# Performance work log

Hardware: AMD Instinct MI355X
Metric: run time of the kernel (lower is better)

## Reference

```python
import jax, jax.numpy as jnp
import numpy as np
from jax import lax

SEQ_LEN = 15
LATENT = 16
HIDDEN = 64
OUT = 1
BATCH = 65536


def setup_inputs() -> dict:
    key = jax.random.key(0)
    ks = jax.random.split(key, 11)
    s = lambda *shape: 1.0 / np.sqrt(HIDDEN)
    def u(k, shape):
        return jax.random.uniform(k, shape, jnp.float32, -1.0 / np.sqrt(HIDDEN), 1.0 / np.sqrt(HIDDEN))
    return {
        "z": jax.random.normal(ks[0], (BATCH, LATENT), jnp.float32),
        "Wih0": u(ks[1], (4 * HIDDEN, LATENT)),
        "Whh0": u(ks[2], (4 * HIDDEN, HIDDEN)),
        "bih0": u(ks[3], (4 * HIDDEN,)),
        "bhh0": u(ks[4], (4 * HIDDEN,)),
        "Wih1": u(ks[5], (4 * HIDDEN, HIDDEN)),
        "Whh1": u(ks[6], (4 * HIDDEN, HIDDEN)),
        "bih1": u(ks[7], (4 * HIDDEN,)),
        "bhh1": u(ks[8], (4 * HIDDEN,)),
        "Wfc": u(ks[9], (OUT, HIDDEN)),
        "bfc": u(ks[10], (OUT,)),
    }


def lstm_layer(x, Wih, Whh, bih, bhh):
    # x: [B, T, D]. PyTorch gate order: i, f, g, o.
    B, T, _ = x.shape
    H = Whh.shape[1]
    # precompute input projections for all timesteps: [T, B, 4H]
    x_proj = jnp.einsum('btd,gd->tbg', x, Wih) + (bih + bhh)

    def step(carry, xp):
        h, c = carry
        gates = xp + h @ Whh.T
        i, f, g, o = jnp.split(gates, 4, axis=-1)
        i = jax.nn.sigmoid(i)
        f = jax.nn.sigmoid(f)
        g = jnp.tanh(g)
        o = jax.nn.sigmoid(o)
        c = f * c + i * g
        h = o * jnp.tanh(c)
        return (h, c), h

    h0 = jnp.zeros((B, H), x.dtype)
    _, ys = lax.scan(step, (h0, h0), x_proj)  # ys: [T, B, H]
    return jnp.swapaxes(ys, 0, 1)  # [B, T, H]


def reference(z, Wih0, Whh0, bih0, bhh0, Wih1, Whh1, bih1, bhh1, Wfc, bfc):
    # z: [B, latent] -> repeat along time: [B, T, latent]
    x = jnp.broadcast_to(z[:, None, :], (z.shape[0], SEQ_LEN, z.shape[1]))
    h1 = lstm_layer(x, Wih0, Whh0, bih0, bhh0)
    # (inter-layer dropout is inactive in eval mode)
    h2 = lstm_layer(h1, Wih1, Whh1, bih1, bhh1)
    return h2 @ Wfc.T + bfc  # [B, T, OUT]
```

## Files before the change

kernel.cpp:

```cpp
#include <hip/hip_runtime.h>

#define TSTEPS 15
#define HID    64
#define LAT    16
#define NBATCH 65536

typedef _Float16 v8h __attribute__((ext_vector_type(8)));
typedef _Float16 v4h __attribute__((ext_vector_type(4)));
typedef float    v4f __attribute__((ext_vector_type(4)));

__device__ __forceinline__ float fast_sig(float x) {
    return __builtin_amdgcn_rcpf(1.0f + __expf(-x));
}
__device__ __forceinline__ float fast_tanh(float x) {
    return 2.0f * __builtin_amdgcn_rcpf(1.0f + __expf(-2.0f * x)) - 1.0f;
}

__device__ __forceinline__ v8h vzero8() {
    v8h v;
#pragma unroll
    for (int i = 0; i < 8; ++i) v[i] = (_Float16)0.0f;
    return v;
}

__global__ __launch_bounds__(512, 2) void lstm2_fused2(
        const float* __restrict__ z,
        const float* __restrict__ Wih0, const float* __restrict__ Whh0,
        const float* __restrict__ bih0, const float* __restrict__ bhh0,
        const float* __restrict__ Wih1, const float* __restrict__ Whh1,
        const float* __restrict__ bih1, const float* __restrict__ bhh1,
        const float* __restrict__ Wfc,  const float* __restrict__ bfc,
        float* __restrict__ out)
{
    __shared__ __align__(16) _Float16 wf[7 * 16 * 64 * 8];
    __shared__ __align__(16) float    bsum[512];
    __shared__ __align__(16) float    wfcs[64];
    __shared__ __align__(16) _Float16 state[8][32 * 72];

    const int tid  = threadIdx.x;
    const int wave = tid >> 6;
    const int lane = tid & 63;
    const int q    = lane >> 4;
    const int c    = lane & 15;
    const int row0 = blockIdx.x * 256 + wave * 32;

#pragma unroll 4
    for (int e = tid; e < 7 * 16 * 64 * 8; e += 512) {
        const int j  = e & 7;
        const int lm = (e >> 3) & 63;
        const int mt = (e >> 9) & 15;
        const int p  = e >> 13;
        const int g  = mt * 16 + (lm & 15);
        const int kk = (lm >> 4) * 8 + j;
        float v;
        if (p == 0)      v = (kk < LAT) ? Wih0[g * LAT + kk] : 0.0f;
        else if (p == 1) v = Whh0[g * HID + kk];
        else if (p == 2) v = Whh0[g * HID + 32 + kk];
        else if (p == 3) v = Wih1[g * HID + kk];
        else if (p == 4) v = Wih1[g * HID + 32 + kk];
        else if (p == 5) v = Whh1[g * HID + kk];
        else             v = Whh1[g * HID + 32 + kk];
        wf[e] = (_Float16)v;
    }
    bsum[tid] = (tid < 256) ? bih0[tid] + bhh0[tid]
                            : bih1[tid - 256] + bhh1[tid - 256];
    if (tid < 64) wfcs[tid] = Wfc[tid];
    __syncthreads();

    _Float16* stW = &state[wave][0];
    const float bfcv = bfc[0];

    v8h zfrag[2];
#pragma unroll
    for (int n = 0; n < 2; ++n) {
        zfrag[n] = vzero8();
        if (q < 2) {
            const float* zp = z + (size_t)(row0 + 16 * n + c) * LAT + q * 8;
            const float4 za = *(const float4*)(zp);
            const float4 zb = *(const float4*)(zp + 4);
            zfrag[n][0] = (_Float16)za.x; zfrag[n][1] = (_Float16)za.y;
            zfrag[n][2] = (_Float16)za.z; zfrag[n][3] = (_Float16)za.w;
            zfrag[n][4] = (_Float16)zb.x; zfrag[n][5] = (_Float16)zb.y;
            zfrag[n][6] = (_Float16)zb.z; zfrag[n][7] = (_Float16)zb.w;
        }
    }

    v8h hf[2][2], gf[2][2];
    float c0s[2][16], c1s[2][16];
#pragma unroll
    for (int n = 0; n < 2; ++n) {
        hf[n][0] = vzero8(); hf[n][1] = vzero8();
        gf[n][0] = vzero8(); gf[n][1] = vzero8();
#pragma unroll
        for (int i = 0; i < 16; ++i) { c0s[n][i] = 0.0f; c1s[n][i] = 0.0f; }
    }

#define AFRAG(pl, mt) (*(const v8h*)&wf[(((pl) * 16 + (mt)) * 64 + lane) * 8])

#pragma unroll 1
    for (int t = 0; t < TSTEPS; ++t) {
        __asm__ __volatile__("" ::: "memory");

#pragma unroll
        for (int a = 0; a < 4; ++a) {
            v4f acc[2][4];
#pragma unroll
            for (int ty = 0; ty < 4; ++ty) {
                const int mt = 4 * ty + a;
                const v4f b  = *(const v4f*)&bsum[64 * ty + 16 * a + 4 * q];
                const v8h a0 = AFRAG(0, mt);
                const v8h a1 = AFRAG(1, mt);
                const v8h a2 = AFRAG(2, mt);
                v4f t0 = __builtin_amdgcn_mfma_f32_16x16x32_f16(a0, zfrag[0], b, 0, 0, 0);
                v4f t1 = __builtin_amdgcn_mfma_f32_16x16x32_f16(a0, zfrag[1], b, 0, 0, 0);
                t0 = __builtin_amdgcn_mfma_f32_16x16x32_f16(a1, hf[0][0], t0, 0, 0, 0);
                t1 = __builtin_amdgcn_mfma_f32_16x16x32_f16(a1, hf[1][0], t1, 0, 0, 0);
                t0 = __builtin_amdgcn_mfma_f32_16x16x32_f16(a2, hf[0][1], t0, 0, 0, 0);
                t1 = __builtin_amdgcn_mfma_f32_16x16x32_f16(a2, hf[1][1], t1, 0, 0, 0);
                acc[0][ty] = t0;
                acc[1][ty] = t1;
            }
#pragma unroll
            for (int n = 0; n < 2; ++n) {
                v4h pk;
#pragma unroll
                for (int r = 0; r < 4; ++r) {
                    const float ig = fast_sig(acc[0][0][r] * 0.0f + ((const v4f*)acc[n])[0][r]);
                    (void)ig;
                }
#pragma unroll
                for (int r = 0; r < 4; ++r) {
                    const float ig = fast_sig(((v4f*)acc[n])[0][r]);
                    const float fg = fast_sig(((v4f*)acc[n])[1][r]);
                    const float gg = fast_tanh(((v4f*)acc[n])[2][r]);
                    const float og = fast_sig(((v4f*)acc[n])[3][r]);
                    const float cc = fg * c0s[n][a * 4 + r] + ig * gg;
                    c0s[n][a * 4 + r] = cc;
                    pk[r] = (_Float16)(og * fast_tanh(cc));
                }
                *(v4h*)&stW[(c + 16 * n) * 72 + 16 * a + 4 * q] = pk;
            }
        }
#pragma unroll
        for (int n = 0; n < 2; ++n) {
            hf[n][0] = *(const v8h*)&stW[(c + 16 * n) * 72 + 8 * q];
            hf[n][1] = *(const v8h*)&stW[(c + 16 * n) * 72 + 32 + 8 * q];
        }

        float p0 = 0.0f, p1 = 0.0f;
#pragma unroll
        for (int a = 0; a < 4; ++a) {
            v4f acc[2][4];
#pragma unroll
            for (int ty = 0; ty < 4; ++ty) {
                const int mt = 4 * ty + a;
                const v4f b  = *(const v4f*)&bsum[256 + 64 * ty + 16 * a + 4 * q];
                const v8h a3 = AFRAG(3, mt);
                const v8h a4 = AFRAG(4, mt);
                const v8h a5 = AFRAG(5, mt);
                const v8h a6 = AFRAG(6, mt);
                v4f t0 = __builtin_amdgcn_mfma_f32_16x16x32_f16(a3, hf[0][0], b, 0, 0, 0);
                v4f t1 = __builtin_amdgcn_mfma_f32_16x16x32_f16(a3, hf[1][0], b, 0, 0, 0);
                t0 = __builtin_amdgcn_mfma_f32_16x16x32_f16(a4, hf[0][1], t0, 0, 0, 0);
                t1 = __builtin_amdgcn_mfma_f32_16x16x32_f16(a4, hf[1][1], t1, 0, 0, 0);
                t0 = __builtin_amdgcn_mfma_f32_16x16x32_f16(a5, gf[0][0], t0, 0, 0, 0);
                t1 = __builtin_amdgcn_mfma_f32_16x16x32_f16(a5, gf[1][0], t1, 0, 0, 0);
                t0 = __builtin_amdgcn_mfma_f32_16x16x32_f16(a6, gf[0][1], t0, 0, 0, 0);
                t1 = __builtin_amdgcn_mfma_f32_16x16x32_f16(a6, gf[1][1], t1, 0, 0, 0);
                acc[0][ty] = t0;
                acc[1][ty] = t1;
            }
            const v4f wv = *(const v4f*)&wfcs[16 * a + 4 * q];
#pragma unroll
            for (int n = 0; n < 2; ++n) {
                v4h pk;
#pragma unroll
                for (int r = 0; r < 4; ++r) {
                    const float ig = fast_sig(((v4f*)acc[n])[0][r]);
                    const float fg = fast_sig(((v4f*)acc[n])[1][r]);
                    const float gg = fast_tanh(((v4f*)acc[n])[2][r]);
                    const float og = fast_sig(((v4f*)acc[n])[3][r]);
                    const float cc = fg * c1s[n][a * 4 + r] + ig * gg;
                    c1s[n][a * 4 + r] = cc;
                    const float hh = og * fast_tanh(cc);
                    pk[r] = (_Float16)hh;
                    if (n == 0) p0 = fmaf(hh, wv[r], p0);
                    else        p1 = fmaf(hh, wv[r], p1);
                }
                *(v4h*)&stW[(c + 16 * n) * 72 + 16 * a + 4 * q] = pk;
            }
        }
#pragma unroll
        for (int n = 0; n < 2; ++n) {
            gf[n][0] = *(const v8h*)&stW[(c + 16 * n) * 72 + 8 * q];
            gf[n][1] = *(const v8h*)&stW[(c + 16 * n) * 72 + 32 + 8 * q];
        }

        p0 += __shfl_xor(p0, 16); p0 += __shfl_xor(p0, 32);
        p1 += __shfl_xor(p1, 16); p1 += __shfl_xor(p1, 32);
        if (lane < 16) {
            out[(size_t)(row0 + lane) * TSTEPS + t]      = p0 + bfcv;
            out[(size_t)(row0 + 16 + lane) * TSTEPS + t] = p1 + bfcv;
        }
    }
#undef AFRAG
}

extern "C" void kernel_launch(void* const* d_in, const int* in_sizes, int n_in,
                              void* d_out, int out_size, void* d_ws, size_t ws_size,
                              hipStream_t stream)
{
    (void)in_sizes; (void)n_in; (void)out_size; (void)d_ws; (void)ws_size;

    const float* z    = (const float*)d_in[0];
    const float* Wih0 = (const float*)d_in[1];
    const float* Whh0 = (const float*)d_in[2];
    const float* bih0 = (const float*)d_in[3];
    const float* bhh0 = (const float*)d_in[4];
    const float* Wih1 = (const float*)d_in[5];
    const float* Whh1 = (const float*)d_in[6];
    const float* bih1 = (const float*)d_in[7];
    const float* bhh1 = (const float*)d_in[8];
    const float* Wfc  = (const float*)d_in[9];
    const float* bfc  = (const float*)d_in[10];

    lstm2_fused2<<<dim3(NBATCH / 256), dim3(512), 0, stream>>>(
        z, Wih0, Whh0, bih0, bhh0, Wih1, Whh1, bih1, bhh1, Wfc, bfc,
        (float*)d_out);
}
```

Baseline: 274.9 us.

## Software-pipeline LSTM layers across timesteps and fold bias and FC into MFMA

The two LSTM layers are skewed by one timestep, so layer 0 at step t and layer 1 at step t-1 run in the same loop iteration. Their independent MFMA chains and activations can then interleave and hide latency. The layer-0 bias is folded into the Wih0 weight fragment through a constant-one column in z, and the output projection now runs as two MFMAs instead of a shuffle reduction. The change raises register pressure (two accumulator sets plus packed h1 values) and adds one extra loop iteration. The f16 conversion now uses packed round-toward-zero, which slightly changes rounding.

```diff
diff --git a/kernel.cpp b/kernel.cpp
--- a/kernel.cpp
+++ b/kernel.cpp
@@ -7,6 +7,7 @@
 
 typedef _Float16 v8h __attribute__((ext_vector_type(8)));
 typedef _Float16 v4h __attribute__((ext_vector_type(4)));
+typedef _Float16 v2h __attribute__((ext_vector_type(2)));
 typedef float    v4f __attribute__((ext_vector_type(4)));
 
 __device__ __forceinline__ float fast_sig(float x) {
@@ -23,7 +24,13 @@
     return v;
 }
 
-__global__ __launch_bounds__(512, 2) void lstm2_fused2(
+__device__ __forceinline__ v4h pack4(float a, float b, float c, float d) {
+    const v2h lo = __builtin_bit_cast(v2h, __builtin_amdgcn_cvt_pkrtz(a, b));
+    const v2h hi = __builtin_bit_cast(v2h, __builtin_amdgcn_cvt_pkrtz(c, d));
+    return __builtin_shufflevector(lo, hi, 0, 1, 2, 3);
+}
+
+__global__ __launch_bounds__(512, 2) void lstm2_pipe(
         const float* __restrict__ z,
         const float* __restrict__ Wih0, const float* __restrict__ Whh0,
         const float* __restrict__ bih0, const float* __restrict__ bhh0,
@@ -33,8 +40,8 @@
         float* __restrict__ out)
 {
     __shared__ __align__(16) _Float16 wf[7 * 16 * 64 * 8];
-    __shared__ __align__(16) float    bsum[512];
-    __shared__ __align__(16) float    wfcs[64];
+    __shared__ __align__(16) _Float16 wfcf[2 * 64 * 8];
+    __shared__ __align__(16) float    bsum1[256];
     __shared__ __align__(16) _Float16 state[8][32 * 72];
 
     const int tid  = threadIdx.x;
@@ -53,7 +60,8 @@
         const int g  = mt * 16 + (lm & 15);
         const int kk = (lm >> 4) * 8 + j;
         float v;
-        if (p == 0)      v = (kk < LAT) ? Wih0[g * LAT + kk] : 0.0f;
+        if (p == 0)      v = (kk < LAT) ? Wih0[g * LAT + kk]
+                           : (kk == LAT ? bih0[g] + bhh0[g] : 0.0f);
         else if (p == 1) v = Whh0[g * HID + kk];
         else if (p == 2) v = Whh0[g * HID + 32 + kk];
         else if (p == 3) v = Wih1[g * HID + kk];
@@ -62,9 +70,15 @@
         else             v = Whh1[g * HID + 32 + kk];
         wf[e] = (_Float16)v;
     }
-    bsum[tid] = (tid < 256) ? bih0[tid] + bhh0[tid]
-                            : bih1[tid - 256] + bhh1[tid - 256];
-    if (tid < 64) wfcs[tid] = Wfc[tid];
+#pragma unroll
+    for (int e = tid; e < 2 * 64 * 8; e += 512) {
+        const int j  = e & 7;
+        const int lm = (e >> 3) & 63;
+        const int kc = e >> 9;
+        const int kk = kc * 32 + (lm >> 4) * 8 + j;
+        wfcf[e] = ((lm & 15) == 0) ? (_Float16)Wfc[kk] : (_Float16)0.0f;
+    }
+    if (tid < 256) bsum1[tid] = bih1[tid] + bhh1[tid];
     __syncthreads();
 
     _Float16* stW = &state[wave][0];
@@ -83,9 +97,11 @@
             zfrag[n][4] = (_Float16)zb.x; zfrag[n][5] = (_Float16)zb.y;
             zfrag[n][6] = (_Float16)zb.z; zfrag[n][7] = (_Float16)zb.w;
         }
+        if (q == 2) zfrag[n][0] = (_Float16)1.0f;
     }
 
     v8h hf[2][2], gf[2][2];
+    v4h h1pk[4][2];
     float c0s[2][16], c1s[2][16];
 #pragma unroll
     for (int n = 0; n < 2; ++n) {
@@ -96,114 +112,119 @@
     }
 
 #define AFRAG(pl, mt) (*(const v8h*)&wf[(((pl) * 16 + (mt)) * 64 + lane) * 8])
+#define MFMA16(A, B, C) __builtin_amdgcn_mfma_f32_16x16x32_f16((A), (B), (C), 0, 0, 0)
 
 #pragma unroll 1
-    for (int t = 0; t < TSTEPS; ++t) {
+    for (int tt = 0; tt <= TSTEPS; ++tt) {
         __asm__ __volatile__("" ::: "memory");
 
+        const bool do_l0 = (tt < TSTEPS);
+        const bool do_l1 = (tt > 0);
+
 #pragma unroll
         for (int a = 0; a < 4; ++a) {
-            v4f acc[2][4];
-#pragma unroll
-            for (int ty = 0; ty < 4; ++ty) {
-                const int mt = 4 * ty + a;
-                const v4f b  = *(const v4f*)&bsum[64 * ty + 16 * a + 4 * q];
-                const v8h a0 = AFRAG(0, mt);
-                const v8h a1 = AFRAG(1, mt);
-                const v8h a2 = AFRAG(2, mt);
-                v4f t0 = __builtin_amdgcn_mfma_f32_16x16x32_f16(a0, zfrag[0], b, 0, 0, 0);
-                v4f t1 = __builtin_amdgcn_mfma_f32_16x16x32_f16(a0, zfrag[1], b, 0, 0, 0);
-                t0 = __builtin_amdgcn_mfma_f32_16x16x32_f16(a1, hf[0][0], t0, 0, 0, 0);
-                t1 = __builtin_amdgcn_mfma_f32_16x16x32_f16(a1, hf[1][0], t1, 0, 0, 0);
-                t0 = __builtin_amdgcn_mfma_f32_16x16x32_f16(a2, hf[0][1], t0, 0, 0, 0);
-                t1 = __builtin_amdgcn_mfma_f32_16x16x32_f16(a2, hf[1][1], t1, 0, 0, 0);
-                acc[0][ty] = t0;
-                acc[1][ty] = t1;
-            }
+            v4f acc0[2][4], acc1[2][4];
+            if (do_l0) {
+#pragma unroll
+                for (int ty = 0; ty < 4; ++ty) {
+                    const int mt = 4 * ty + a;
+                    const v8h a0 = AFRAG(0, mt);
+                    const v8h a1 = AFRAG(1, mt);
+                    const v8h a2 = AFRAG(2, mt);
+                    v4f t0 = {0.f, 0.f, 0.f, 0.f};
+                    v4f t1 = {0.f, 0.f, 0.f, 0.f};
+                    t0 = MFMA16(a0, zfrag[0], t0);  t1 = MFMA16(a0, zfrag[1], t1);
+                    t0 = MFMA16(a1, hf[0][0], t0);  t1 = MFMA16(a1, hf[1][0], t1);
+                    t0 = MFMA16(a2, hf[0][1], t0);  t1 = MFMA16(a2, hf[1][1], t1);
+                    acc0[0][ty] = t0;  acc0[1][ty] = t1;
+                }
+            }
+            if (do_l1) {
+#pragma unroll
+                for (int ty = 0; ty < 4; ++ty) {
+                    const int mt = 4 * ty + a;
+                    const v4f b  = *(const v4f*)&bsum1[64 * ty + 16 * a + 4 * q];
+                    const v8h a3 = AFRAG(3, mt);
+                    const v8h a4 = AFRAG(4, mt);
+                    const v8h a5 = AFRAG(5, mt);
+                    const v8h a6 = AFRAG(6, mt);
+                    v4f t0 = MFMA16(a3, hf[0][0], b);
+                    v4f t1 = MFMA16(a3, hf[1][0], b);
+                    t0 = MFMA16(a4, hf[0][1], t0);  t1 = MFMA16(a4, hf[1][1], t1);
+                    t0 = MFMA16(a5, gf[0][0], t0);  t1 = MFMA16(a5, gf[1][0], t1);
+                    t0 = MFMA16(a6, gf[0][1], t0);  t1 = MFMA16(a6, gf[1][1], t1);
+                    acc1[0][ty] = t0;  acc1[1][ty] = t1;
+                }
+            }
+            if (do_l0) {
+#pragma unroll
+                for (int n = 0; n < 2; ++n) {
+                    float hh[4];
+#pragma unroll
+                    for (int r = 0; r < 4; ++r) {
+                        const float ig = fast_sig(acc0[n][0][r]);
+                        const float fg = fast_sig(acc0[n][1][r]);
+                        const float gg = fast_tanh(acc0[n][2][r]);
+                        const float og = fast_sig(acc0[n][3][r]);
+                        const float cc = fg * c0s[n][a * 4 + r] + ig * gg;
+                        c0s[n][a * 4 + r] = cc;
+                        hh[r] = og * fast_tanh(cc);
+                    }
+                    *(v4h*)&stW[(c + 16 * n) * 72 + 16 * a + 4 * q] =
+                        pack4(hh[0], hh[1], hh[2], hh[3]);
+                }
+            }
+            if (do_l1) {
+#pragma unroll
+                for (int n = 0; n < 2; ++n) {
+                    float hh[4];
+#pragma unroll
+                    for (int r = 0; r < 4; ++r) {
+                        const float ig = fast_sig(acc1[n][0][r]);
+                        const float fg = fast_sig(acc1[n][1][r]);
+                        const float gg = fast_tanh(acc1[n][2][r]);
+                        const float og = fast_sig(acc1[n][3][r]);
+                        const float cc = fg * c1s[n][a * 4 + r] + ig * gg;
+                        c1s[n][a * 4 + r] = cc;
+                        hh[r] = og * fast_tanh(cc);
+                    }
+                    h1pk[a][n] = pack4(hh[0], hh[1], hh[2], hh[3]);
+                }
+            }
+        }
+
+        if (do_l0) {
 #pragma unroll
             for (int n = 0; n < 2; ++n) {
-                v4h pk;
-#pragma unroll
-                for (int r = 0; r < 4; ++r) {
-                    const float ig = fast_sig(acc[0][0][r] * 0.0f + ((const v4f*)acc[n])[0][r]);
-                    (void)ig;
-                }
-#pragma unroll
-                for (int r = 0; r < 4; ++r) {
-                    const float ig = fast_sig(((v4f*)acc[n])[0][r]);
-                    const float fg = fast_sig(((v4f*)acc[n])[1][r]);
-                    const float gg = fast_tanh(((v4f*)acc[n])[2][r]);
-                    const float og = fast_sig(((v4f*)acc[n])[3][r]);
-                    const float cc = fg * c0s[n][a * 4 + r] + ig * gg;
-                    c0s[n][a * 4 + r] = cc;
-                    pk[r] = (_Float16)(og * fast_tanh(cc));
-                }
-                *(v4h*)&stW[(c + 16 * n) * 72 + 16 * a + 4 * q] = pk;
-            }
-        }
-#pragma unroll
-        for (int n = 0; n < 2; ++n) {
-            hf[n][0] = *(const v8h*)&stW[(c + 16 * n) * 72 + 8 * q];
-            hf[n][1] = *(const v8h*)&stW[(c + 16 * n) * 72 + 32 + 8 * q];
-        }
-
-        float p0 = 0.0f, p1 = 0.0f;
-#pragma unroll
-        for (int a = 0; a < 4; ++a) {
-            v4f acc[2][4];
-#pragma unroll
-            for (int ty = 0; ty < 4; ++ty) {
-                const int mt = 4 * ty + a;
-                const v4f b  = *(const v4f*)&bsum[256 + 64 * ty + 16 * a + 4 * q];
-                const v8h a3 = AFRAG(3, mt);
-                const v8h a4 = AFRAG(4, mt);
-                const v8h a5 = AFRAG(5, mt);
-                const v8h a6 = AFRAG(6, mt);
-                v4f t0 = __builtin_amdgcn_mfma_f32_16x16x32_f16(a3, hf[0][0], b, 0, 0, 0);
-                v4f t1 = __builtin_amdgcn_mfma_f32_16x16x32_f16(a3, hf[1][0], b, 0, 0, 0);
-                t0 = __builtin_amdgcn_mfma_f32_16x16x32_f16(a4, hf[0][1], t0, 0, 0, 0);
-                t1 = __builtin_amdgcn_mfma_f32_16x16x32_f16(a4, hf[1][1], t1, 0, 0, 0);
-                t0 = __builtin_amdgcn_mfma_f32_16x16x32_f16(a5, gf[0][0], t0, 0, 0, 0);
-                t1 = __builtin_amdgcn_mfma_f32_16x16x32_f16(a5, gf[1][0], t1, 0, 0, 0);
-                t0 = __builtin_amdgcn_mfma_f32_16x16x32_f16(a6, gf[0][1], t0, 0, 0, 0);
-                t1 = __builtin_amdgcn_mfma_f32_16x16x32_f16(a6, gf[1][1], t1, 0, 0, 0);
-                acc[0][ty] = t0;
-                acc[1][ty] = t1;
-            }
-            const v4f wv = *(const v4f*)&wfcs[16 * a + 4 * q];
+                hf[n][0] = *(const v8h*)&stW[(c + 16 * n) * 72 + 8 * q];
+                hf[n][1] = *(const v8h*)&stW[(c + 16 * n) * 72 + 32 + 8 * q];
+            }
+        }
+        if (do_l1) {
+#pragma unroll
+            for (int a = 0; a < 4; ++a)
+#pragma unroll
+                for (int n = 0; n < 2; ++n)
+                    *(v4h*)&stW[(c + 16 * n) * 72 + 16 * a + 4 * q] = h1pk[a][n];
 #pragma unroll
             for (int n = 0; n < 2; ++n) {
-                v4h pk;
-#pragma unroll
-                for (int r = 0; r < 4; ++r) {
-                    const float ig = fast_sig(((v4f*)acc[n])[0][r]);
-                    const float fg = fast_sig(((v4f*)acc[n])[1][r]);
-                    const float gg = fast_tanh(((v4f*)acc[n])[2][r]);
-                    const float og = fast_sig(((v4f*)acc[n])[3][r]);
-                    const float cc = fg * c1s[n][a * 4 + r] + ig * gg;
-                    c1s[n][a * 4 + r] = cc;
-                    const float hh = og * fast_tanh(cc);
-                    pk[r] = (_Float16)hh;
-                    if (n == 0) p0 = fmaf(hh, wv[r], p0);
-                    else        p1 = fmaf(hh, wv[r], p1);
-                }
-                *(v4h*)&stW[(c + 16 * n) * 72 + 16 * a + 4 * q] = pk;
-            }
-        }
-#pragma unroll
-        for (int n = 0; n < 2; ++n) {
-            gf[n][0] = *(const v8h*)&stW[(c + 16 * n) * 72 + 8 * q];
-            gf[n][1] = *(const v8h*)&stW[(c + 16 * n) * 72 + 32 + 8 * q];
-        }
-
-        p0 += __shfl_xor(p0, 16); p0 += __shfl_xor(p0, 32);
-        p1 += __shfl_xor(p1, 16); p1 += __shfl_xor(p1, 32);
-        if (lane < 16) {
-            out[(size_t)(row0 + lane) * TSTEPS + t]      = p0 + bfcv;
-            out[(size_t)(row0 + 16 + lane) * TSTEPS + t] = p1 + bfcv;
+                gf[n][0] = *(const v8h*)&stW[(c + 16 * n) * 72 + 8 * q];
+                gf[n][1] = *(const v8h*)&stW[(c + 16 * n) * 72 + 32 + 8 * q];
+            }
+            const v8h w0 = *(const v8h*)&wfcf[(0 * 64 + lane) * 8];
+            const v8h w1 = *(const v8h*)&wfcf[(1 * 64 + lane) * 8];
+#pragma unroll
+            for (int n = 0; n < 2; ++n) {
+                v4f f = {0.f, 0.f, 0.f, 0.f};
+                f = MFMA16(w0, gf[n][0], f);
+                f = MFMA16(w1, gf[n][1], f);
+                if (lane < 16)
+                    out[(size_t)(row0 + 16 * n + lane) * TSTEPS + (tt - 1)] = f[0] + bfcv;
+            }
         }
     }
 #undef AFRAG
+#undef MFMA16
 }
 
 extern "C" void kernel_launch(void* const* d_in, const int* in_sizes, int n_in,
@@ -224,7 +245,7 @@
     const float* Wfc  = (const float*)d_in[9];
     const float* bfc  = (const float*)d_in[10];
 
-    lstm2_fused2<<<dim3(NBATCH / 256), dim3(512), 0, stream>>>(
+    lstm2_pipe<<<dim3(NBATCH / 256), dim3(512), 0, stream>>>(
         z, Wih0, Whh0, bih0, bhh0, Wih1, Whh1, bih1, bhh1, Wfc, bfc,
         (float*)d_out);
 }
```

After: 282.1 us. 1.03x slower.
